# Performance work log

Hardware: AMD Instinct MI355X
Metric: run time of the kernel (lower is better)

Reference implementation:

```python
import jax, jax.numpy as jnp
import numpy as np

DIM = 1024
HEADS = 16
HEAD_DIM = DIM // HEADS
EPS = 1e-5


def _layer_norm(z, g, b):
    m = jnp.mean(z, axis=-1, keepdims=True)
    v = jnp.var(z, axis=-1, keepdims=True)
    return (z - m) * jax.lax.rsqrt(v + EPS) * g + b


def setup_inputs() -> dict:
    key = jax.random.key(0)
    ks = jax.random.split(key, 8)
    B, T, S = 2, 2048, 2048
    x = jax.random.normal(ks[0], (B, T, DIM), dtype=jnp.float32)
    context = jax.random.normal(ks[1], (B, S, DIM), dtype=jnp.float32)
    w_qkv = jax.random.normal(ks[2], (DIM, 3 * DIM), dtype=jnp.float32) * 0.02
    b_qkv = jnp.zeros((3 * DIM,), dtype=jnp.float32)
    w_out = jax.random.normal(ks[3], (DIM, DIM), dtype=jnp.float32) * 0.02
    b_out = jnp.zeros((DIM,), dtype=jnp.float32)
    ln_g = jnp.ones((DIM,), dtype=jnp.float32)
    ln_b = jnp.zeros((DIM,), dtype=jnp.float32)
    return {"x": x, "context": context, "w_qkv": w_qkv, "b_qkv": b_qkv,
            "w_out": w_out, "b_out": b_out, "ln_g": ln_g, "ln_b": ln_b}


def reference(x, context, w_qkv, b_qkv, w_out, b_out, ln_g, ln_b):
    B, T, C = x.shape
    S = context.shape[1]
    scale = HEAD_DIM ** -0.5

    def split_heads(z):  # [B, L, C] -> [B, H, L, Dh]
        return z.reshape(z.shape[0], z.shape[1], HEADS, HEAD_DIM).transpose(0, 2, 1, 3)

    # self qkv
    qkv = _layer_norm(x, ln_g, ln_b) @ w_qkv + b_qkv  # [B, T, 3C]
    q = split_heads(qkv[..., :C])
    k = split_heads(qkv[..., C:2 * C])
    v = split_heads(qkv[..., 2 * C:])

    # context k, v from the shared qkv projection (K/V slices)
    ckv = _layer_norm(context, ln_g, ln_b) @ w_qkv + b_qkv  # [B, S, 3C]
    ck = split_heads(ckv[..., C:2 * C])
    cv = split_heads(ckv[..., 2 * C:])

    k = jnp.concatenate([k, ck], axis=2)  # [B, H, T+S, Dh]
    v = jnp.concatenate([v, cv], axis=2)

    attn = jax.nn.softmax(jnp.einsum('bhtd,bhsd->bhts', q, k) * scale, axis=-1)
    out = jnp.einsum('bhts,bhsd->bhtd', attn, v)  # [B, H, T, Dh]
    out = out.transpose(0, 2, 1, 3).reshape(B, T, C)
    return out @ w_out + b_out + x
```

## Files before the change

### kernel.cpp

```cpp
#include <hip/hip_runtime.h>
#include <stdint.h>

#define H 16
#define DH 64
#define T 2048
#define SS 2048
#define L 4096
#define DIM 1024
#define BB 2

typedef __bf16 bf16x8 __attribute__((ext_vector_type(8)));
typedef float f32x4 __attribute__((ext_vector_type(4)));
typedef float f32x16 __attribute__((ext_vector_type(16)));
typedef unsigned u32x4 __attribute__((ext_vector_type(4)));

__device__ __forceinline__ unsigned short f2bf(float f){
  unsigned u = __builtin_bit_cast(unsigned, f);
  u += 0x7fff + ((u >> 16) & 1);
  return (unsigned short)(u >> 16);
}

__device__ __forceinline__ unsigned cvt_pk_bf16(float lo, float hi){
  unsigned r;
  asm("v_cvt_pk_bf16_f32 %0, %1, %2" : "=v"(r) : "v"(lo), "v"(hi));
  return r;
}

__device__ __forceinline__ float fmax3(float a, float b, float c){
  float r;
  asm("v_max3_f32 %0, %1, %2, %3" : "=v"(r) : "v"(a), "v"(b), "v"(c));
  return r;
}

__device__ __forceinline__ void gload_lds16(const void* g, void* l){
  void* gnc = const_cast<void*>(g);
  __builtin_amdgcn_global_load_lds((__attribute__((address_space(1))) void*)gnc,
                                   (__attribute__((address_space(3))) void*)l, 16, 0, 0);
}

__global__ __launch_bounds__(256) void ln_kernel(const float* __restrict__ x, const float* __restrict__ ctx,
                          const float* __restrict__ g, const float* __restrict__ b,
                          unsigned short* __restrict__ out){
  int row = blockIdx.x;
  int tid = threadIdx.x;
  const float* src = (row < BB*T) ? (x + (size_t)row*DIM) : (ctx + (size_t)(row - BB*T)*DIM);
  float4 v = reinterpret_cast<const float4*>(src)[tid];
  float s  = v.x + v.y + v.z + v.w;
  float s2 = v.x*v.x + v.y*v.y + v.z*v.z + v.w*v.w;
  #pragma unroll
  for (int off = 32; off > 0; off >>= 1){
    s  += __shfl_down(s,  off, 64);
    s2 += __shfl_down(s2, off, 64);
  }
  __shared__ float red[8];
  if ((tid & 63) == 0){ red[(tid>>6)*2] = s; red[(tid>>6)*2+1] = s2; }
  __syncthreads();
  s  = red[0] + red[2] + red[4] + red[6];
  s2 = red[1] + red[3] + red[5] + red[7];
  float mean = s * (1.0f/DIM);
  float var  = s2 * (1.0f/DIM) - mean*mean;
  float rstd = rsqrtf(var + 1e-5f);
  float4 gg = reinterpret_cast<const float4*>(g)[tid];
  float4 bv = reinterpret_cast<const float4*>(b)[tid];
  ushort4 o;
  o.x = f2bf((v.x-mean)*rstd*gg.x + bv.x);
  o.y = f2bf((v.y-mean)*rstd*gg.y + bv.y);
  o.z = f2bf((v.z-mean)*rstd*gg.z + bv.z);
  o.w = f2bf((v.w-mean)*rstd*gg.w + bv.w);
  reinterpret_cast<ushort4*>(out + (size_t)row*DIM)[tid] = o;
}

__global__ __launch_bounds__(256) void transpose_f32_bf16(const float* __restrict__ in,
                          unsigned short* __restrict__ out, int R, int C){
  __shared__ float tile[32][33];
  int c0 = blockIdx.x*32, r0 = blockIdx.y*32;
  int tx = threadIdx.x & 31, ty = threadIdx.x >> 5;
  #pragma unroll
  for (int k = 0; k < 4; k++)
    tile[ty + k*8][tx] = in[(size_t)(r0 + ty + k*8)*C + c0 + tx];
  __syncthreads();
  #pragma unroll
  for (int k = 0; k < 4; k++)
    out[(size_t)(c0 + ty + k*8)*R + r0 + tx] = f2bf(tile[tx][ty + k*8]);
}

__global__ __launch_bounds__(64) void zero_ctr(unsigned* __restrict__ c){
  if (threadIdx.x == 0) *c = 0u;
}

__global__ __launch_bounds__(256) void qkv_gemm(const unsigned short* __restrict__ A,
      const unsigned short* __restrict__ Bt, const float* __restrict__ bias,
      unsigned short* __restrict__ qbuf, unsigned short* __restrict__ kbuf,
      unsigned short* __restrict__ vtbuf, unsigned* __restrict__ ctr){
  __shared__ union {
    struct { unsigned short at[2][128*32]; unsigned short bt[2][128*32]; } s;
    unsigned short ct[128][136];
    unsigned short vt[128][136];
  } u;
  __shared__ unsigned s_g;
  int tid = threadIdx.x, lane = tid & 63, wv = tid >> 6;
  int wm = (wv >> 1)*64, wn = (wv & 1)*64;

  for (;;){
    if (tid == 0) s_g = atomicAdd(ctr, 1u);
    __syncthreads();
    unsigned g = s_g;
    if (g >= 1280u) return;
    int xcd = g & 7, a = g >> 3;
    int w = (a < 32) ? ((a >> 2)*8 + (a & 3)) : (a + 32);
    int mblk = ((w & 7) << 3) + xcd;
    int nblk = w >> 3;
    int n0 = nblk*128, m0 = mblk*128;

    f32x4 acc[4][4];
    #pragma unroll
    for (int i = 0; i < 4; i++)
      #pragma unroll
      for (int j = 0; j < 4; j++) acc[i][j] = (f32x4){0.f,0.f,0.f,0.f};

    #define QSTAGE(bufi, k0) { \
      _Pragma("unroll") \
      for (int c = 0; c < 2; c++){ \
        int idx = c*256 + tid; \
        int row = idx >> 2, koff = (idx & 3)*16; \
        gload_lds16((const char*)A  + ((size_t)(m0+row)*DIM + (k0))*2 + koff, \
                    (char*)u.s.at[bufi] + (c*256 + wv*64)*16); \
        gload_lds16((const char*)Bt + ((size_t)(n0+row)*DIM + (k0))*2 + koff, \
                    (char*)u.s.bt[bufi] + (c*256 + wv*64)*16); \
      } }

    QSTAGE(0, 0);
    __syncthreads();

    for (int kt = 0; kt < 32; kt++){
      int bufi = kt & 1;
      if (kt + 1 < 32) QSTAGE(bufi^1, (kt+1)*32);
      bf16x8 af[4], bfv[4];
      #pragma unroll
      for (int i = 0; i < 4; i++){
        af[i]  = *reinterpret_cast<const bf16x8*>((const char*)u.s.at[bufi] + (wm + i*16 + (lane&15))*64 + (lane>>4)*16);
        bfv[i] = *reinterpret_cast<const bf16x8*>((const char*)u.s.bt[bufi] + (wn + i*16 + (lane&15))*64 + (lane>>4)*16);
      }
      #pragma unroll
      for (int mi = 0; mi < 4; mi++)
        #pragma unroll
        for (int ni = 0; ni < 4; ni++)
          acc[mi][ni] = __builtin_amdgcn_mfma_f32_16x16x32_bf16(af[mi], bfv[ni], acc[mi][ni], 0,0,0);
      __syncthreads();
    }

    int sec = n0 >> 10;
    if (sec < 2){
      float scale = (sec == 0) ? 0.18033688f : 1.0f;
      #pragma unroll
      for (int ni = 0; ni < 4; ni++){
        int nl = wn + ni*16 + (lane & 15);
        float bv = bias[n0 + nl];
        #pragma unroll
        for (int mi = 0; mi < 4; mi++){
          int ml = wm + mi*16 + ((lane >> 4) << 2);
          #pragma unroll
          for (int r = 0; r < 4; r++)
            u.ct[ml + r][nl] = f2bf((acc[mi][ni][r] + bv)*scale);
        }
      }
      __syncthreads();
      #pragma unroll
      for (int c = 0; c < 8; c++){
        int idx = c*256 + tid;
        int row = idx >> 4, ch = idx & 15;
        bf16x8 v = *reinterpret_cast<const bf16x8*>(&u.ct[row][ch*8]);
        int gm = m0 + row, gn = n0 + ch*8;
        int cc = gn & 1023, hh2 = cc >> 6, d = cc & 63;
        bool isctx = gm >= BB*T;
        int rm = isctx ? gm - BB*T : gm;
        int bidx = rm >> 11, tt = rm & 2047;
        size_t bh2 = (size_t)bidx*H + hh2;
        if (sec == 0){
          *reinterpret_cast<bf16x8*>(qbuf + (bh2*T + tt)*DH + d) = v;
        } else {
          int j = isctx ? T + tt : tt;
          *reinterpret_cast<bf16x8*>(kbuf + (bh2*L + j)*DH + d) = v;
        }
      }
    } else {
      #pragma unroll
      for (int ni = 0; ni < 4; ni++){
        int nl = wn + ni*16 + (lane & 15);
        float bv = bias[n0 + nl];
        #pragma unroll
        for (int mi = 0; mi < 4; mi++){
          int ml = wm + mi*16 + ((lane >> 4) << 2);
          ushort4 o;
          o.x = f2bf(acc[mi][ni][0] + bv);
          o.y = f2bf(acc[mi][ni][1] + bv);
          o.z = f2bf(acc[mi][ni][2] + bv);
          o.w = f2bf(acc[mi][ni][3] + bv);
          *reinterpret_cast<ushort4*>(&u.vt[nl][ml]) = o;
        }
      }
      __syncthreads();
      #pragma unroll
      for (int c = 0; c < 8; c++){
        int idx = c*256 + tid;
        int nl = idx >> 4, ch = idx & 15;
        bf16x8 v = *reinterpret_cast<const bf16x8*>(&u.vt[nl][ch*8]);
        int gn = n0 + nl;
        int cc = gn & 1023, hh2 = cc >> 6, d = cc & 63;
        int gm = m0 + ch*8;
        bool isctx = gm >= BB*T;
        int rm = isctx ? gm - BB*T : gm;
        int bidx = rm >> 11, tt = rm & 2047;
        int j = isctx ? T + tt : tt;
        size_t bh2 = (size_t)bidx*H + hh2;
        *reinterpret_cast<bf16x8*>(vtbuf + (bh2*DH + d)*L + j) = v;
      }
    }
    __syncthreads();
  }
}

__global__ __launch_bounds__(256, 4) void attn_kernel(const unsigned short* __restrict__ q,
      const unsigned short* __restrict__ kbuf, const unsigned short* __restrict__ vtbuf,
      unsigned short* __restrict__ obuf, float* __restrict__ mbuf, float* __restrict__ lbuf){
  int hw = blockIdx.x;
  int wid = (hw & 7)*128 + (hw >> 3);
  int qt = wid & 15, bh = (wid >> 4) & 31, cb = wid >> 9;
  int hh = bh & 15, b = bh >> 4;
  int tid = threadIdx.x, lane = tid & 63, wv = tid >> 6;
  int hi = lane >> 5, q32 = lane & 31;
  __shared__ unsigned short kt[2][64*64];
  __shared__ unsigned short vtt[2][64*64];
  size_t bhs = (size_t)b*H + hh;
  int qbase = qt*128 + wv*32;

  const unsigned short* qp = q + (bhs*T + qbase + q32)*DH + hi*8;
  bf16x8 qf[4];
  #pragma unroll
  for (int ks = 0; ks < 4; ks++)
    qf[ks] = *reinterpret_cast<const bf16x8*>(qp + ks*16);

  bf16x8 ones;
  #pragma unroll
  for (int j = 0; j < 8; j++) ones[j] = (__bf16)1.0f;

  f32x16 o_acc[2], l_vec;
  #pragma unroll
  for (int d = 0; d < 2; d++)
    #pragma unroll
    for (int i = 0; i < 16; i++) o_acc[d][i] = 0.f;
  #pragma unroll
  for (int i = 0; i < 16; i++) l_vec[i] = 0.f;
  float m_l = -1e30f;

  const char* kg = (const char*)(kbuf + bhs*(size_t)L*DH) + (size_t)cb*2048*128;
  const char* vg = (const char*)(vtbuf + bhs*(size_t)DH*L) + (size_t)cb*4096;

  #define STAGE(bufi, jt) { \
    _Pragma("unroll") \
    for (int c = 0; c < 2; c++){ \
      int idx = c*256 + tid; \
      int row = idx >> 3, c16 = idx & 7; \
      int sc16 = c16 ^ (row & 7); \
      gload_lds16(kg + (size_t)((jt)*64 + row)*128 + sc16*16, \
                  (char*)kt[bufi] + (c*256 + wv*64)*16); \
      gload_lds16(vg + (size_t)row*(L*2) + (jt)*128 + sc16*16, \
                  (char*)vtt[bufi] + (c*256 + wv*64)*16); \
    } }

  STAGE(0, 0);
  __syncthreads();

  for (int jt = 0; jt < 32; ++jt){
    int bufi = jt & 1;
    if (jt + 1 < 32) STAGE(bufi^1, jt+1);
    const char* kb = (const char*)kt[bufi];
    const char* vb = (const char*)vtt[bufi];

    f32x16 sc[2];
    #pragma unroll
    for (int t = 0; t < 2; t++)
      #pragma unroll
      for (int i = 0; i < 16; i++) sc[t][i] = 0.f;
    #pragma unroll
    for (int ks = 0; ks < 4; ks++){
      #pragma unroll
      for (int t = 0; t < 2; t++){
        int row = t*32 + q32;
        bf16x8 kf = *reinterpret_cast<const bf16x8*>(kb + row*128 + (((ks*2+hi) ^ (row&7))*16));
        sc[t] = __builtin_amdgcn_mfma_f32_32x32x16_bf16(kf, qf[ks], sc[t], 0,0,0);
      }
    }

    float rt[2];
    #pragma unroll
    for (int t = 0; t < 2; t++){
      float v0 = fmax3(sc[t][0],  sc[t][1],  sc[t][2]);
      float v1 = fmax3(sc[t][3],  sc[t][4],  sc[t][5]);
      float v2 = fmax3(sc[t][6],  sc[t][7],  sc[t][8]);
      float v3 = fmax3(sc[t][9],  sc[t][10], sc[t][11]);
      float v4 = fmax3(sc[t][12], sc[t][13], sc[t][14]);
      rt[t] = fmaxf(fmax3(v0, v1, v2), fmax3(v3, v4, sc[t][15]));
    }
    float tm = fmaxf(rt[0], rt[1]);

    if (!__all(tm - m_l <= 8.0f)){
      float tmf = fmaxf(tm, __shfl_xor(tm, 32, 64));
      float mn = fmaxf(m_l, tmf);
      float alpha = __builtin_amdgcn_exp2f(m_l - mn);
      m_l = mn;
      #pragma unroll
      for (int d = 0; d < 2; d++)
        #pragma unroll
        for (int i = 0; i < 16; i++) o_acc[d][i] *= alpha;
      l_vec[0] *= alpha;
    }
    #pragma unroll
    for (int t = 0; t < 2; t++)
      #pragma unroll
      for (int i = 0; i < 16; i++)
        sc[t][i] = __builtin_amdgcn_exp2f(sc[t][i] - m_l);

    bf16x8 pfrag[4];
    #pragma unroll
    for (int t = 0; t < 2; t++){
      #pragma unroll
      for (int half = 0; half < 2; half++){
        unsigned p01 = cvt_pk_bf16(sc[t][half*8+0], sc[t][half*8+1]);
        unsigned p23 = cvt_pk_bf16(sc[t][half*8+2], sc[t][half*8+3]);
        unsigned p45 = cvt_pk_bf16(sc[t][half*8+4], sc[t][half*8+5]);
        unsigned p67 = cvt_pk_bf16(sc[t][half*8+6], sc[t][half*8+7]);
        asm("v_permlane32_swap_b32 %0, %1" : "+v"(p01), "+v"(p45));
        asm("v_permlane32_swap_b32 %0, %1" : "+v"(p23), "+v"(p67));
        u32x4 w = (u32x4){p01, p23, p45, p67};
        pfrag[t*2 + half] = __builtin_bit_cast(bf16x8, w);
      }
    }

    #pragma unroll
    for (int ks = 0; ks < 4; ks++){
      #pragma unroll
      for (int d = 0; d < 2; d++){
        int row = d*32 + q32;
        bf16x8 vf = *reinterpret_cast<const bf16x8*>(vb + row*128 + (((ks*2+hi) ^ (row&7))*16));
        o_acc[d] = __builtin_amdgcn_mfma_f32_32x32x16_bf16(vf, pfrag[ks], o_acc[d], 0,0,0);
      }
      l_vec = __builtin_amdgcn_mfma_f32_32x32x16_bf16(ones, pfrag[ks], l_vec, 0,0,0);
    }
    __syncthreads();
  }

  float inv = 1.0f / l_vec[0];
  unsigned short* aop = obuf + (size_t)cb*BB*H*T*DH + ((size_t)bh*T + qbase + q32)*DH;
  #pragma unroll
  for (int d = 0; d < 2; d++)
    #pragma unroll
    for (int rg = 0; rg < 4; rg++){
      int d0 = d*32 + rg*8 + hi*4;
      ushort4 o;
      o.x = __builtin_bit_cast(unsigned short, (__bf16)(o_acc[d][rg*4+0]*inv));
      o.y = __builtin_bit_cast(unsigned short, (__bf16)(o_acc[d][rg*4+1]*inv));
      o.z = __builtin_bit_cast(unsigned short, (__bf16)(o_acc[d][rg*4+2]*inv));
      o.w = __builtin_bit_cast(unsigned short, (__bf16)(o_acc[d][rg*4+3]*inv));
      *reinterpret_cast<ushort4*>(aop + d0) = o;
    }
  if (hi == 0){
    size_t mi = ((size_t)cb*BB*H + bh)*T + qbase + q32;
    mbuf[mi] = m_l;
    lbuf[mi] = l_vec[0];
  }
}

__global__ __launch_bounds__(256) void attn_combine(const unsigned short* __restrict__ obuf,
      const float* __restrict__ mbuf, const float* __restrict__ lbuf,
      unsigned short* __restrict__ ao){
  int gid = blockIdx.x*256 + threadIdx.x;
  int d8 = gid & 7;
  int qg = gid >> 3;
  int qq = qg & (T-1);
  int bh = qg >> 11;
  int b = bh >> 4, h = bh & 15;
  float m0 = mbuf[(size_t)qg];
  float m1 = mbuf[(size_t)BB*H*T + qg];
  float l0 = lbuf[(size_t)qg];
  float l1 = lbuf[(size_t)BB*H*T + qg];
  float mm = fmaxf(m0, m1);
  float w0 = l0 * __builtin_amdgcn_exp2f(m0 - mm);
  float w1 = l1 * __builtin_amdgcn_exp2f(m1 - mm);
  float inv = 1.0f / (w0 + w1);
  w0 *= inv; w1 *= inv;
  bf16x8 o0 = *reinterpret_cast<const bf16x8*>(obuf + (size_t)qg*DH + d8*8);
  bf16x8 o1 = *reinterpret_cast<const bf16x8*>(obuf + (size_t)BB*H*T*DH + (size_t)qg*DH + d8*8);
  bf16x8 res;
  #pragma unroll
  for (int j = 0; j < 8; j++)
    res[j] = (__bf16)(w0*(float)o0[j] + w1*(float)o1[j]);
  *reinterpret_cast<bf16x8*>(ao + ((size_t)b*T + qq)*DIM + h*DH + d8*8) = res;
}

__global__ __launch_bounds__(256) void out_gemm(const unsigned short* __restrict__ A,
      const unsigned short* __restrict__ Bt, const float* __restrict__ bout,
      const float* __restrict__ xres, float* __restrict__ out){
  int n0 = blockIdx.x*128, m0 = blockIdx.y*64;
  __shared__ unsigned short at[2][64*32];
  __shared__ unsigned short btile[2][128*32];
  int tid = threadIdx.x, lane = tid & 63, wv = tid >> 6;
  int wm = (wv >> 1)*32, wn = (wv & 1)*64;
  f32x4 acc[2][4];
  #pragma unroll
  for (int i = 0; i < 2; i++)
    #pragma unroll
    for (int j = 0; j < 4; j++) acc[i][j] = (f32x4){0.f,0.f,0.f,0.f};

  #define OSTAGE(bufi, k0) { \
    { int row = tid >> 2, koff = (tid & 3)*16; \
      gload_lds16((const char*)A + ((size_t)(m0+row)*DIM + (k0))*2 + koff, \
                  (char*)at[bufi] + (wv*64)*16); } \
    _Pragma("unroll") \
    for (int c = 0; c < 2; c++){ \
      int idx = c*256 + tid; \
      int row = idx >> 2, koff = (idx & 3)*16; \
      gload_lds16((const char*)Bt + ((size_t)(n0+row)*DIM + (k0))*2 + koff, \
                  (char*)btile[bufi] + (c*256 + wv*64)*16); \
    } }

  OSTAGE(0, 0);
  __syncthreads();

  for (int kt = 0; kt < 32; kt++){
    int bufi = kt & 1;
    if (kt + 1 < 32) OSTAGE(bufi^1, (kt+1)*32);
    bf16x8 af[2], bfv[4];
    #pragma unroll
    for (int i = 0; i < 2; i++)
      af[i]  = *reinterpret_cast<const bf16x8*>((const char*)at[bufi] + (wm + i*16 + (lane&15))*64 + (lane>>4)*16);
    #pragma unroll
    for (int i = 0; i < 4; i++)
      bfv[i] = *reinterpret_cast<const bf16x8*>((const char*)btile[bufi] + (wn + i*16 + (lane&15))*64 + (lane>>4)*16);
    #pragma unroll
    for (int mi = 0; mi < 2; mi++)
      #pragma unroll
      for (int ni = 0; ni < 4; ni++)
        acc[mi][ni] = __builtin_amdgcn_mfma_f32_16x16x32_bf16(af[mi], bfv[ni], acc[mi][ni], 0,0,0);
    __syncthreads();
  }

  #pragma unroll
  for (int ni = 0; ni < 4; ni++){
    int gn = n0 + wn + ni*16 + (lane & 15);
    float bv = bout[gn];
    #pragma unroll
    for (int mi = 0; mi < 2; mi++){
      int gmb = m0 + wm + mi*16 + ((lane >> 4) << 2);
      #pragma unroll
      for (int r = 0; r < 4; r++){
        int gm = gmb + r;
        out[(size_t)gm*DIM + gn] = acc[mi][ni][r] + bv + xres[(size_t)gm*DIM + gn];
      }
    }
  }
}

extern "C" void kernel_launch(void* const* d_in, const int* in_sizes, int n_in,
                              void* d_out, int out_size, void* d_ws, size_t ws_size,
                              hipStream_t stream){
  const float* x    = (const float*)d_in[0];
  const float* ctx  = (const float*)d_in[1];
  const float* wqkv = (const float*)d_in[2];
  const float* bqkv = (const float*)d_in[3];
  const float* wout = (const float*)d_in[4];
  const float* bout = (const float*)d_in[5];
  const float* lng  = (const float*)d_in[6];
  const float* lnb  = (const float*)d_in[7];
  float* out = (float*)d_out;

  char* ws = (char*)d_ws;
  unsigned short* wqkvT  = (unsigned short*)ws; ws += (size_t)3072*1024*2;
  unsigned short* woutT  = (unsigned short*)ws; ws += (size_t)1024*1024*2;
  unsigned short* ln_all = (unsigned short*)ws; ws += (size_t)8192*1024*2;
  unsigned short* qbuf   = (unsigned short*)ws; ws += (size_t)BB*H*T*DH*2;
  unsigned short* kbuf   = (unsigned short*)ws; ws += (size_t)BB*H*L*DH*2;
  unsigned short* vtbuf  = (unsigned short*)ws; ws += (size_t)BB*H*DH*L*2;
  unsigned short* aobuf  = (unsigned short*)ws; ws += (size_t)BB*T*DIM*2;

  unsigned short* obuf = ln_all;
  float* mbuf = (float*)wqkvT;
  float* lbuf = mbuf + (size_t)2*BB*H*T;
  unsigned* qctr = (unsigned*)aobuf;

  transpose_f32_bf16<<<dim3(3072/32, 1024/32), dim3(256), 0, stream>>>(wqkv, wqkvT, 1024, 3072);
  transpose_f32_bf16<<<dim3(1024/32, 1024/32), dim3(256), 0, stream>>>(wout, woutT, 1024, 1024);
  ln_kernel<<<dim3(8192), dim3(256), 0, stream>>>(x, ctx, lng, lnb, ln_all);
  zero_ctr<<<dim3(1), dim3(64), 0, stream>>>(qctr);
  qkv_gemm<<<dim3(1024), dim3(256), 0, stream>>>(ln_all, wqkvT, bqkv, qbuf, kbuf, vtbuf, qctr);
  attn_kernel<<<dim3(1024), dim3(256), 0, stream>>>(qbuf, kbuf, vtbuf, obuf, mbuf, lbuf);
  attn_combine<<<dim3(BB*H*T*8/256), dim3(256), 0, stream>>>(obuf, mbuf, lbuf, aobuf);
  out_gemm<<<dim3(1024/128, 4096/64), dim3(256), 0, stream>>>(aobuf, woutT, bout, x, out);
}
```

Baseline: 240.8 us.

## Replace persistent atomic tile scheduler in QKV GEMM with direct grid launch

The QKV GEMM drops its persistent loop, which fetched tiles through a global atomic counter, and now launches one block per tile (1280 blocks), so the zero_ctr kernel is no longer needed. The epilogue staging buffer in LDS is halved by writing the output in two 64-row passes, so the union shrinks to the size of the double-buffered operand tiles. Launch bounds now ask for 5 blocks per CU. This removes the atomic and its barrier and should let more blocks fit on each CU, at the cost of extra barriers in the epilogue and relying on the hardware block scheduler for load balance.

After: 211.7 us, median of 2. 1.14x faster.

```diff
diff --git a/kernel.cpp b/kernel.cpp
--- a/kernel.cpp
+++ b/kernel.cpp
@@ -84,93 +84,87 @@
     out[(size_t)(c0 + ty + k*8)*R + r0 + tx] = f2bf(tile[tx][ty + k*8]);
 }
 
-__global__ __launch_bounds__(64) void zero_ctr(unsigned* __restrict__ c){
-  if (threadIdx.x == 0) *c = 0u;
-}
-
-__global__ __launch_bounds__(256) void qkv_gemm(const unsigned short* __restrict__ A,
+__global__ __launch_bounds__(256, 5) void qkv_gemm(const unsigned short* __restrict__ A,
       const unsigned short* __restrict__ Bt, const float* __restrict__ bias,
       unsigned short* __restrict__ qbuf, unsigned short* __restrict__ kbuf,
-      unsigned short* __restrict__ vtbuf, unsigned* __restrict__ ctr){
+      unsigned short* __restrict__ vtbuf){
+  int g = blockIdx.x;
+  int xcd = g & 7, a = g >> 3;
+  int w = (a < 32) ? ((a >> 2)*8 + (a & 3)) : (a + 32);
+  int mblk = ((w & 7) << 3) + xcd;
+  int nblk = w >> 3;
+  int n0 = nblk*128, m0 = mblk*128;
   __shared__ union {
     struct { unsigned short at[2][128*32]; unsigned short bt[2][128*32]; } s;
-    unsigned short ct[128][136];
-    unsigned short vt[128][136];
+    unsigned short ct[64][136];
+    unsigned short vt[128][72];
   } u;
-  __shared__ unsigned s_g;
   int tid = threadIdx.x, lane = tid & 63, wv = tid >> 6;
   int wm = (wv >> 1)*64, wn = (wv & 1)*64;
-
-  for (;;){
-    if (tid == 0) s_g = atomicAdd(ctr, 1u);
+  f32x4 acc[4][4];
+  #pragma unroll
+  for (int i = 0; i < 4; i++)
+    #pragma unroll
+    for (int j = 0; j < 4; j++) acc[i][j] = (f32x4){0.f,0.f,0.f,0.f};
+
+  #define QSTAGE(bufi, k0) { \
+    _Pragma("unroll") \
+    for (int c = 0; c < 2; c++){ \
+      int idx = c*256 + tid; \
+      int row = idx >> 2, koff = (idx & 3)*16; \
+      gload_lds16((const char*)A  + ((size_t)(m0+row)*DIM + (k0))*2 + koff, \
+                  (char*)u.s.at[bufi] + (c*256 + wv*64)*16); \
+      gload_lds16((const char*)Bt + ((size_t)(n0+row)*DIM + (k0))*2 + koff, \
+                  (char*)u.s.bt[bufi] + (c*256 + wv*64)*16); \
+    } }
+
+  QSTAGE(0, 0);
+  __syncthreads();
+
+  for (int kt = 0; kt < 32; kt++){
+    int bufi = kt & 1;
+    if (kt + 1 < 32) QSTAGE(bufi^1, (kt+1)*32);
+    bf16x8 af[4], bfv[4];
+    #pragma unroll
+    for (int i = 0; i < 4; i++){
+      af[i]  = *reinterpret_cast<const bf16x8*>((const char*)u.s.at[bufi] + (wm + i*16 + (lane&15))*64 + (lane>>4)*16);
+      bfv[i] = *reinterpret_cast<const bf16x8*>((const char*)u.s.bt[bufi] + (wn + i*16 + (lane&15))*64 + (lane>>4)*16);
+    }
+    #pragma unroll
+    for (int mi = 0; mi < 4; mi++)
+      #pragma unroll
+      for (int ni = 0; ni < 4; ni++)
+        acc[mi][ni] = __builtin_amdgcn_mfma_f32_16x16x32_bf16(af[mi], bfv[ni], acc[mi][ni], 0,0,0);
     __syncthreads();
-    unsigned g = s_g;
-    if (g >= 1280u) return;
-    int xcd = g & 7, a = g >> 3;
-    int w = (a < 32) ? ((a >> 2)*8 + (a & 3)) : (a + 32);
-    int mblk = ((w & 7) << 3) + xcd;
-    int nblk = w >> 3;
-    int n0 = nblk*128, m0 = mblk*128;
-
-    f32x4 acc[4][4];
-    #pragma unroll
-    for (int i = 0; i < 4; i++)
-      #pragma unroll
-      for (int j = 0; j < 4; j++) acc[i][j] = (f32x4){0.f,0.f,0.f,0.f};
-
-    #define QSTAGE(bufi, k0) { \
-      _Pragma("unroll") \
-      for (int c = 0; c < 2; c++){ \
-        int idx = c*256 + tid; \
-        int row = idx >> 2, koff = (idx & 3)*16; \
-        gload_lds16((const char*)A  + ((size_t)(m0+row)*DIM + (k0))*2 + koff, \
-                    (char*)u.s.at[bufi] + (c*256 + wv*64)*16); \
-        gload_lds16((const char*)Bt + ((size_t)(n0+row)*DIM + (k0))*2 + koff, \
-                    (char*)u.s.bt[bufi] + (c*256 + wv*64)*16); \
-      } }
-
-    QSTAGE(0, 0);
-    __syncthreads();
-
-    for (int kt = 0; kt < 32; kt++){
-      int bufi = kt & 1;
-      if (kt + 1 < 32) QSTAGE(bufi^1, (kt+1)*32);
-      bf16x8 af[4], bfv[4];
-      #pragma unroll
-      for (int i = 0; i < 4; i++){
-        af[i]  = *reinterpret_cast<const bf16x8*>((const char*)u.s.at[bufi] + (wm + i*16 + (lane&15))*64 + (lane>>4)*16);
-        bfv[i] = *reinterpret_cast<const bf16x8*>((const char*)u.s.bt[bufi] + (wn + i*16 + (lane&15))*64 + (lane>>4)*16);
-      }
-      #pragma unroll
-      for (int mi = 0; mi < 4; mi++)
+  }
+
+  int sec = n0 >> 10;
+  if (sec < 2){
+    float scale = (sec == 0) ? 0.18033688f : 1.0f;
+    #pragma unroll
+    for (int p = 0; p < 2; p++){
+      __syncthreads();
+      if ((wv >> 1) == p){
         #pragma unroll
-        for (int ni = 0; ni < 4; ni++)
-          acc[mi][ni] = __builtin_amdgcn_mfma_f32_16x16x32_bf16(af[mi], bfv[ni], acc[mi][ni], 0,0,0);
+        for (int ni = 0; ni < 4; ni++){
+          int nl = wn + ni*16 + (lane & 15);
+          float bv = bias[n0 + nl];
+          #pragma unroll
+          for (int mi = 0; mi < 4; mi++){
+            int mloc = mi*16 + ((lane >> 4) << 2);
+            #pragma unroll
+            for (int r = 0; r < 4; r++)
+              u.ct[mloc + r][nl] = f2bf((acc[mi][ni][r] + bv)*scale);
+          }
+        }
+      }
       __syncthreads();
-    }
-
-    int sec = n0 >> 10;
-    if (sec < 2){
-      float scale = (sec == 0) ? 0.18033688f : 1.0f;
-      #pragma unroll
-      for (int ni = 0; ni < 4; ni++){
-        int nl = wn + ni*16 + (lane & 15);
-        float bv = bias[n0 + nl];
-        #pragma unroll
-        for (int mi = 0; mi < 4; mi++){
-          int ml = wm + mi*16 + ((lane >> 4) << 2);
-          #pragma unroll
-          for (int r = 0; r < 4; r++)
-            u.ct[ml + r][nl] = f2bf((acc[mi][ni][r] + bv)*scale);
-        }
-      }
-      __syncthreads();
-      #pragma unroll
-      for (int c = 0; c < 8; c++){
+      #pragma unroll
+      for (int c = 0; c < 4; c++){
         int idx = c*256 + tid;
         int row = idx >> 4, ch = idx & 15;
         bf16x8 v = *reinterpret_cast<const bf16x8*>(&u.ct[row][ch*8]);
-        int gm = m0 + row, gn = n0 + ch*8;
+        int gm = m0 + p*64 + row, gn = n0 + ch*8;
         int cc = gn & 1023, hh2 = cc >> 6, d = cc & 63;
         bool isctx = gm >= BB*T;
         int rm = isctx ? gm - BB*T : gm;
@@ -183,31 +177,37 @@
           *reinterpret_cast<bf16x8*>(kbuf + (bh2*L + j)*DH + d) = v;
         }
       }
-    } else {
-      #pragma unroll
-      for (int ni = 0; ni < 4; ni++){
-        int nl = wn + ni*16 + (lane & 15);
-        float bv = bias[n0 + nl];
+    }
+  } else {
+    #pragma unroll
+    for (int p = 0; p < 2; p++){
+      __syncthreads();
+      if ((wv >> 1) == p){
         #pragma unroll
-        for (int mi = 0; mi < 4; mi++){
-          int ml = wm + mi*16 + ((lane >> 4) << 2);
-          ushort4 o;
-          o.x = f2bf(acc[mi][ni][0] + bv);
-          o.y = f2bf(acc[mi][ni][1] + bv);
-          o.z = f2bf(acc[mi][ni][2] + bv);
-          o.w = f2bf(acc[mi][ni][3] + bv);
-          *reinterpret_cast<ushort4*>(&u.vt[nl][ml]) = o;
+        for (int ni = 0; ni < 4; ni++){
+          int nl = wn + ni*16 + (lane & 15);
+          float bv = bias[n0 + nl];
+          #pragma unroll
+          for (int mi = 0; mi < 4; mi++){
+            int mloc = mi*16 + ((lane >> 4) << 2);
+            ushort4 o;
+            o.x = f2bf(acc[mi][ni][0] + bv);
+            o.y = f2bf(acc[mi][ni][1] + bv);
+            o.z = f2bf(acc[mi][ni][2] + bv);
+            o.w = f2bf(acc[mi][ni][3] + bv);
+            *reinterpret_cast<ushort4*>(&u.vt[nl][mloc]) = o;
+          }
         }
       }
       __syncthreads();
       #pragma unroll
-      for (int c = 0; c < 8; c++){
+      for (int c = 0; c < 4; c++){
         int idx = c*256 + tid;
-        int nl = idx >> 4, ch = idx & 15;
+        int nl = idx >> 3, ch = idx & 7;
         bf16x8 v = *reinterpret_cast<const bf16x8*>(&u.vt[nl][ch*8]);
         int gn = n0 + nl;
         int cc = gn & 1023, hh2 = cc >> 6, d = cc & 63;
-        int gm = m0 + ch*8;
+        int gm = m0 + p*64 + ch*8;
         bool isctx = gm >= BB*T;
         int rm = isctx ? gm - BB*T : gm;
         int bidx = rm >> 11, tt = rm & 2047;
@@ -216,7 +216,6 @@
         *reinterpret_cast<bf16x8*>(vtbuf + (bh2*DH + d)*L + j) = v;
       }
     }
-    __syncthreads();
   }
 }
 
@@ -486,13 +485,11 @@
   unsigned short* obuf = ln_all;
   float* mbuf = (float*)wqkvT;
   float* lbuf = mbuf + (size_t)2*BB*H*T;
-  unsigned* qctr = (unsigned*)aobuf;
 
   transpose_f32_bf16<<<dim3(3072/32, 1024/32), dim3(256), 0, stream>>>(wqkv, wqkvT, 1024, 3072);
   transpose_f32_bf16<<<dim3(1024/32, 1024/32), dim3(256), 0, stream>>>(wout, woutT, 1024, 1024);
   ln_kernel<<<dim3(8192), dim3(256), 0, stream>>>(x, ctx, lng, lnb, ln_all);
-  zero_ctr<<<dim3(1), dim3(64), 0, stream>>>(qctr);
-  qkv_gemm<<<dim3(1024), dim3(256), 0, stream>>>(ln_all, wqkvT, bqkv, qbuf, kbuf, vtbuf, qctr);
+  qkv_gemm<<<dim3(1280), dim3(256), 0, stream>>>(ln_all, wqkvT, bqkv, qbuf, kbuf, vtbuf);
   attn_kernel<<<dim3(1024), dim3(256), 0, stream>>>(qbuf, kbuf, vtbuf, obuf, mbuf, lbuf);
   attn_combine<<<dim3(BB*H*T*8/256), dim3(256), 0, stream>>>(obuf, mbuf, lbuf, aobuf);
   out_gemm<<<dim3(1024/128, 4096/64), dim3(256), 0, stream>>>(aobuf, woutT, bout, x, out);
```
